# Kernel optimization log

Measured on AMD Instinct MI355X. Metric: run time of the kernel, lower is better.

Reference implementation:

```python
import jax, jax.numpy as jnp
import numpy as np

H = 8
DK = 64          # d_model // h
D_MODEL = 512
DIM_G = 64       # trignometric geometry embedding dim
WAVE_LEN = 1000.0


def box_relational_embedding(boxes):
    # boxes: [B, N, 4] = (x_min, y_min, x_max, y_max)
    x_min, y_min, x_max, y_max = [boxes[..., i:i + 1] for i in range(4)]  # each [B,N,1]
    cx = (x_min + x_max) * 0.5
    cy = (y_min + y_max) * 0.5
    w = (x_max - x_min) + 1.0
    h = (y_max - y_min) + 1.0

    def rel(c, s):
        # log(clamp(|c_i - c_j| / s_i, 1e-3)) -> [B,N,N]
        return jnp.log(jnp.clip(jnp.abs((c - jnp.swapaxes(c, -2, -1)) / s), 1e-3, None))

    delta_x = rel(cx, w)
    delta_y = rel(cy, h)
    delta_w = jnp.log(w / jnp.swapaxes(w, -2, -1))
    delta_h = jnp.log(h / jnp.swapaxes(h, -2, -1))
    pos = jnp.stack([delta_x, delta_y, delta_w, delta_h], axis=-1)  # [B,N,N,4]

    n_freq = DIM_G // 8  # 8 frequencies per geometric feature
    feat_range = jnp.arange(n_freq, dtype=pos.dtype)
    dim_mat = 1.0 / (WAVE_LEN ** (feat_range / n_freq))            # [n_freq]
    mul = (100.0 * pos)[..., None] * dim_mat                        # [B,N,N,4,n_freq]
    B, N = pos.shape[0], pos.shape[1]
    mul = mul.reshape(B, N, N, 4 * n_freq)                          # [B,N,N,32]
    return jnp.concatenate([jnp.sin(mul), jnp.cos(mul)], axis=-1)   # [B,N,N,64]


def setup_inputs() -> dict:
    key = jax.random.key(0)
    ks = jax.random.split(key, 14)
    B, N = 4, 512
    s = 0.02
    return {
        "input_query": jax.random.normal(ks[0], (B, N, D_MODEL), jnp.float32),
        "input_key":   jax.random.normal(ks[1], (B, N, D_MODEL), jnp.float32),
        "input_value": jax.random.normal(ks[2], (B, N, D_MODEL), jnp.float32),
        "input_box":   jax.random.uniform(ks[3], (B, N, 4), jnp.float32),
        "Wq": jax.random.normal(ks[4], (D_MODEL, D_MODEL), jnp.float32) * s,
        "bq": jax.random.normal(ks[5], (D_MODEL,), jnp.float32) * s,
        "Wk": jax.random.normal(ks[6], (D_MODEL, D_MODEL), jnp.float32) * s,
        "bk": jax.random.normal(ks[7], (D_MODEL,), jnp.float32) * s,
        "Wv": jax.random.normal(ks[8], (D_MODEL, D_MODEL), jnp.float32) * s,
        "bv": jax.random.normal(ks[9], (D_MODEL,), jnp.float32) * s,
        "Wo": jax.random.normal(ks[10], (D_MODEL, D_MODEL), jnp.float32) * s,
        "bo": jax.random.normal(ks[11], (D_MODEL,), jnp.float32) * s,
        "WG": jax.random.normal(ks[12], (H, DIM_G), jnp.float32) * s,
        "bG": jax.random.normal(ks[13], (H,), jnp.float32) * s,
    }


def reference(input_query, input_key, input_value, input_box,
              Wq, bq, Wk, bk, Wv, bv, Wo, bo, WG, bG):
    B, N, _ = input_query.shape

    # geometry log-bias per head: relu(Linear_h(emb)) -> [B,H,N,N]
    emb = box_relational_embedding(input_box)                        # [B,N,N,64]
    wg = jax.nn.relu(jnp.einsum('bmng,hg->bhmn', emb, WG)
                     + bG[None, :, None, None])

    def proj(x, W, b):
        # torch Linear: x @ W^T + b, then split heads -> [B,H,N,DK]
        y = x @ W.T + b
        return y.reshape(B, N, H, DK).transpose(0, 2, 1, 3)

    q = proj(input_query, Wq, bq)
    k = proj(input_key, Wk, bk)
    v = proj(input_value, Wv, bv)

    scale = 1.0 / jnp.sqrt(jnp.asarray(DK, q.dtype))
    scores = jnp.einsum('bhqd,bhkd->bhqk', q, k) * scale             # [B,H,N,N]
    logits = jnp.log(jnp.clip(wg, 1e-6, None)) + scores
    attn = jax.nn.softmax(logits, axis=-1)                           # dropout is identity in eval
    out = jnp.einsum('bhqk,bhkd->bhqd', attn, v)
    out = out.transpose(0, 2, 1, 3).reshape(B, N, H * DK)
    return out @ Wo.T + bo
```

## Files before the change

### kernel.cpp

```cpp
#include <hip/hip_runtime.h>
#include <hip/hip_bf16.h>
#include <cstdint>

typedef unsigned short u16;
typedef unsigned int u32;
typedef __attribute__((ext_vector_type(8))) short short8;
typedef __attribute__((ext_vector_type(4))) float f32x4;
typedef __attribute__((ext_vector_type(4))) unsigned int u32x4;
typedef __attribute__((ext_vector_type(4))) unsigned short u16x4;

#define REV 15.91549431f

__device__ __forceinline__ u16 f2b(float x) { return __builtin_bit_cast(u16, (__bf16)x); }
__device__ __forceinline__ u16 f2h(float x) { return __builtin_bit_cast(u16, (_Float16)x); }
__device__ __forceinline__ float c_dim_f(int f) {
    const float c[8] = {1.0f, 0.42169650f, 0.17782794f, 0.074989421f,
                        0.031622777f, 0.013335214f, 0.0056234132f, 0.0023713737f};
    return c[f];
}
__device__ __forceinline__ void gload_lds16(const void* g, void* l) {
    __builtin_amdgcn_global_load_lds((const __attribute__((address_space(1))) u32*)g,
                                     (__attribute__((address_space(3))) u32*)l, 16, 0, 0);
}

__global__ __launch_bounds__(256) void prep_k(const float* __restrict__ s0,
                                              const float* __restrict__ s1,
                                              const float* __restrict__ s2,
                                              const float* __restrict__ s3,
                                              const float* __restrict__ s4,
                                              const float* __restrict__ s5,
                                              const float* __restrict__ s6,
                                              const float* __restrict__ box,
                                              const float* __restrict__ WG,
                                              const float* __restrict__ bG,
                                              u16* __restrict__ dstX,
                                              u16* __restrict__ dstW,
                                              u16* __restrict__ outW) {
    __shared__ char embs[256 * 128];
    const int z = blockIdx.z;
    const int t = threadIdx.x;

    if (z < 7) {
        const float* s;
        u16* dst;
        if (z < 3) {
            s = (z == 0) ? s0 : (z == 1) ? s1 : s2;
            dst = dstX + (size_t)z * 1048576;
        } else {
            if (blockIdx.x >= 256) return;
            s = (z == 3) ? s3 : (z == 4) ? s4 : (z == 5) ? s5 : s6;
            dst = dstW + (size_t)(z - 3) * 262144;
        }
        int i = (blockIdx.x * 256 + t) * 4;
        float4 v = *(const float4*)&s[i];
        u16x4 o = { f2b(v.x), f2b(v.y), f2b(v.z), f2b(v.w) };
        *(u16x4*)&dst[i] = o;
        return;
    }

    const int wave = t >> 6, lane = t & 63;
    const int b = z - 7;
    const int jt = blockIdx.x & 1, ii = blockIdx.x >> 1;
    const int j = (jt << 8) + t;
    const int swz = (t & 7) << 4;

    float4 bi = *(const float4*)&box[(size_t)(((b << 9) + ii) << 2)];
    float4 bj = *(const float4*)&box[(size_t)(((b << 9) + j) << 2)];
    float cxi = (bi.x + bi.z) * 0.5f, cyi = (bi.y + bi.w) * 0.5f;
    float wdi = bi.z - bi.x + 1.0f,   hgi = bi.w - bi.y + 1.0f;
    float cxj = (bj.x + bj.z) * 0.5f, cyj = (bj.y + bj.w) * 0.5f;
    float wdj = bj.z - bj.x + 1.0f,   hgj = bj.w - bj.y + 1.0f;

    float pos[4];
    pos[0] = __logf(fmaxf(fabsf((cxi - cxj) / wdi), 1e-3f));
    pos[1] = __logf(fmaxf(fabsf((cyi - cyj) / hgi), 1e-3f));
    pos[2] = __logf(wdi) - __logf(wdj);
    pos[3] = __logf(hgi) - __logf(hgj);

#pragma unroll
    for (int p = 0; p < 4; p++) {
        float rev = pos[p] * REV;
        u32x4 sp, cp;
#pragma unroll
        for (int f = 0; f < 4; f++) {
            float a0 = rev * c_dim_f(2 * f), a1 = rev * c_dim_f(2 * f + 1);
            sp[f] = (u32)f2b(__builtin_amdgcn_sinf(a0)) | ((u32)f2b(__builtin_amdgcn_sinf(a1)) << 16);
            cp[f] = (u32)f2b(__builtin_amdgcn_cosf(a0)) | ((u32)f2b(__builtin_amdgcn_cosf(a1)) << 16);
        }
        *(u32x4*)(embs + (((t << 7) + (p << 4)) ^ swz)) = sp;
        *(u32x4*)(embs + (((t << 7) + 64 + (p << 4)) ^ swz)) = cp;
    }

    const int hh = lane & 15;
    const int ko = (lane >> 4) << 3;
    short8 bf0 = {0,0,0,0,0,0,0,0}, bf1 = {0,0,0,0,0,0,0,0};
    float bGh = 0.0f;
    if (hh < 8) {
        const float* wrow = WG + hh * 64;
#pragma unroll
        for (int e = 0; e < 8; e++) {
            bf0[e] = (short)f2b(wrow[ko + e]);
            bf1[e] = (short)f2b(wrow[32 + ko + e]);
        }
        bGh = bG[hh];
    }
    __syncthreads();

#pragma unroll
    for (int tt = 0; tt < 4; tt++) {
        int mt = (wave << 2) + tt;
        int row = (mt << 4) + hh;
        int rswz = (row & 7) << 4;
        short8 a0v = *(const short8*)(embs + (((row << 7) + (ko << 1)) ^ rswz));
        short8 a1v = *(const short8*)(embs + (((row << 7) + 64 + (ko << 1)) ^ rswz));
        f32x4 acc = {0.f, 0.f, 0.f, 0.f};
        acc = __builtin_amdgcn_mfma_f32_16x16x32_bf16(a0v, bf0, acc, 0, 0, 0);
        acc = __builtin_amdgcn_mfma_f32_16x16x32_bf16(a1v, bf1, acc, 0, 0, 0);
        if (hh < 8) {
            int j0 = (jt << 8) + (mt << 4) + ((lane >> 4) << 2);
            u16x4 ow;
#pragma unroll
            for (int r = 0; r < 4; r++)
                ow[r] = f2h(fmaxf(acc[r] + bGh, 1e-6f) * 1024.0f);
            *(u16x4*)&outW[((size_t)((b << 3) + hh) << 18) + ((size_t)ii << 9) + j0] = ow;
        }
    }
}

__global__ __launch_bounds__(256) void attn_k(const u16* __restrict__ Qb,
                                              const u16* __restrict__ Kb,
                                              const u16* __restrict__ VT,
                                              const u16* __restrict__ Wp,
                                              u16* __restrict__ ATT) {
    __shared__ u16 Pl[4][16 * 68];
    __shared__ float Mrg[3][64][25];
    const int t = threadIdx.x;
    const int wave = t >> 6, lane = t & 63;
    const int c = lane & 15, g = lane >> 4;
    const int bid = blockIdx.x;
    const int qb = bid & 31, bh = bid >> 5;
    const int b = bh >> 3, h = bh & 7;
    const int q0 = qb << 4;

    const u16* Qp = Qb + ((size_t)bh << 15);
    const u16* Kp = Kb + ((size_t)bh << 15);
    const u16* Vp = VT + ((size_t)bh << 15);
    const _Float16* Bp = (const _Float16*)Wp + ((size_t)bh << 18) + ((size_t)q0 << 9);

    short8 qf[2];
#pragma unroll
    for (int ks = 0; ks < 2; ks++)
        qf[ks] = *(const short8*)&Qp[(size_t)(q0 + c) * 64 + ks * 32 + g * 8];

    f32x4 o[4] = {};
    float m[4] = {-1e30f, -1e30f, -1e30f, -1e30f};
    float l[4] = {0.f, 0.f, 0.f, 0.f};

    for (int kt = 0; kt < 2; kt++) {
        const int k0 = ((wave << 1) + kt) << 6;
        short8 kf[4][2], vf[4][2];
#pragma unroll
        for (int jj = 0; jj < 4; jj++)
#pragma unroll
            for (int ks = 0; ks < 2; ks++) {
                kf[jj][ks] = *(const short8*)&Kp[(size_t)(k0 + jj * 16 + c) * 64 + ks * 32 + g * 8];
                vf[jj][ks] = *(const short8*)&Vp[(size_t)(jj * 16 + c) * 512 + k0 + ks * 32 + g * 8];
            }
        float wgt[4][4];
#pragma unroll
        for (int jj = 0; jj < 4; jj++)
#pragma unroll
            for (int r = 0; r < 4; r++)
                wgt[jj][r] = (float)Bp[(size_t)(g * 4 + r) * 512 + k0 + jj * 16 + c];

        f32x4 sa[4] = {};
        __builtin_amdgcn_s_setprio(1);
#pragma unroll
        for (int jj = 0; jj < 4; jj++)
#pragma unroll
            for (int ks = 0; ks < 2; ks++)
                sa[jj] = __builtin_amdgcn_mfma_f32_16x16x32_bf16(qf[ks], kf[jj][ks], sa[jj], 0, 0, 0);
        __builtin_amdgcn_s_setprio(0);

        float s[4][4];
#pragma unroll
        for (int r = 0; r < 4; r++) {
#pragma unroll
            for (int jj = 0; jj < 4; jj++)
                s[jj][r] = sa[jj][r] * 0.125f;
            float v = fmaxf(fmaxf(s[0][r], s[1][r]), fmaxf(s[2][r], s[3][r]));
#pragma unroll
            for (int off = 1; off < 16; off <<= 1)
                v = fmaxf(v, __shfl_xor(v, off));
            float mn = fmaxf(m[r], v);
            float alpha = __expf(m[r] - mn);
            m[r] = mn;
            float rs = 0.f;
#pragma unroll
            for (int jj = 0; jj < 4; jj++) {
                float p = wgt[jj][r] * __expf(s[jj][r] - mn);
                s[jj][r] = p;
                rs += p;
            }
#pragma unroll
            for (int off = 1; off < 16; off <<= 1)
                rs += __shfl_xor(rs, off);
            l[r] = l[r] * alpha + rs;
#pragma unroll
            for (int jjo = 0; jjo < 4; jjo++)
                o[jjo][r] *= alpha;
        }

#pragma unroll
        for (int jj = 0; jj < 4; jj++)
#pragma unroll
            for (int r = 0; r < 4; r++)
                Pl[wave][(g * 4 + r) * 68 + jj * 16 + c] = f2b(s[jj][r]);
        asm volatile("s_waitcnt lgkmcnt(0)" ::: "memory");
        __builtin_amdgcn_sched_barrier(0);

        short8 pa[2];
#pragma unroll
        for (int ks = 0; ks < 2; ks++)
            pa[ks] = *(const short8*)&Pl[wave][c * 68 + ks * 32 + g * 8];
        __builtin_amdgcn_s_setprio(1);
#pragma unroll
        for (int jjo = 0; jjo < 4; jjo++)
#pragma unroll
            for (int ks = 0; ks < 2; ks++)
                o[jjo] = __builtin_amdgcn_mfma_f32_16x16x32_bf16(pa[ks], vf[jjo][ks], o[jjo], 0, 0, 0);
        __builtin_amdgcn_s_setprio(0);
        __builtin_amdgcn_sched_barrier(0);
    }

    if (wave > 0) {
#pragma unroll
        for (int r = 0; r < 4; r++) {
            Mrg[wave - 1][lane][r] = m[r];
            Mrg[wave - 1][lane][4 + r] = l[r];
#pragma unroll
            for (int jjo = 0; jjo < 4; jjo++)
                Mrg[wave - 1][lane][8 + jjo * 4 + r] = o[jjo][r];
        }
    }
    __syncthreads();
    if (wave == 0) {
#pragma unroll
        for (int w = 0; w < 3; w++) {
#pragma unroll
            for (int r = 0; r < 4; r++) {
                float m1 = Mrg[w][lane][r];
                float l1 = Mrg[w][lane][4 + r];
                float mn = fmaxf(m[r], m1);
                float a0 = __expf(m[r] - mn), a1 = __expf(m1 - mn);
                m[r] = mn;
                l[r] = l[r] * a0 + l1 * a1;
#pragma unroll
                for (int jjo = 0; jjo < 4; jjo++)
                    o[jjo][r] = o[jjo][r] * a0 + Mrg[w][lane][8 + jjo * 4 + r] * a1;
            }
        }
#pragma unroll
        for (int r = 0; r < 4; r++) {
            float inv = 1.0f / l[r];
            int row = q0 + g * 4 + r;
#pragma unroll
            for (int jjo = 0; jjo < 4; jjo++)
                ATT[(size_t)(((b << 9) + row) << 9) + (h << 6) + jjo * 16 + c] = f2b(o[jjo][r] * inv);
        }
    }
}

__global__ __launch_bounds__(256) void proj_k(const u16* __restrict__ Xall,
                                              const u16* __restrict__ Wall,
                                              const float* __restrict__ bq,
                                              const float* __restrict__ bk,
                                              const float* __restrict__ bv,
                                              u16* __restrict__ Qb,
                                              u16* __restrict__ Kb,
                                              u16* __restrict__ VT) {
    __shared__ u16 As[2][64 * 32];
    __shared__ u16 Bs[2][64 * 32];

    const int t = threadIdx.x;
    const int wave = t >> 6, lane = t & 63;
    const int wr = wave >> 1, wc = wave & 1;
    const int m0 = blockIdx.y * 64, n0 = blockIdx.x * 64;
    const int z = blockIdx.z;

    const u16* A  = Xall + (size_t)z * 1048576;
    const u16* Bm = Wall + (size_t)z * 262144;
    const float* bias = (z == 0) ? bq : (z == 1) ? bk : bv;
    u16* out = (z == 0) ? Qb : (z == 1) ? Kb : VT;

    f32x4 acc[2][2] = {};
    const int srow = t >> 2;
    const int scol = (((t & 3) ^ ((t >> 3) & 3)) << 3);
    const int c = lane & 15, g = lane >> 4;
    const int gsw = (g ^ ((c >> 1) & 3)) << 3;

    const size_t arow = (size_t)(m0 + srow) * 512 + scol;
    const size_t brow = (size_t)(n0 + srow) * 512 + scol;

    gload_lds16(&A[arow], &As[0][t * 8]);
    gload_lds16(&Bm[brow], &Bs[0][t * 8]);

    int cur = 0;
    for (int k0 = 0; k0 < 512; k0 += 32, cur ^= 1) {
        if (k0 + 32 < 512) {
            gload_lds16(&A[arow + k0 + 32], &As[cur ^ 1][t * 8]);
            gload_lds16(&Bm[brow + k0 + 32], &Bs[cur ^ 1][t * 8]);
            asm volatile("s_waitcnt vmcnt(2)" ::: "memory");
        } else {
            asm volatile("s_waitcnt vmcnt(0)" ::: "memory");
        }
        __builtin_amdgcn_s_barrier();
        __builtin_amdgcn_sched_barrier(0);
        short8 af[2], bfr[2];
#pragma unroll
        for (int i = 0; i < 2; i++)
            af[i] = *(const short8*)&As[cur][(wr * 32 + i * 16 + c) * 32 + gsw];
#pragma unroll
        for (int jj = 0; jj < 2; jj++)
            bfr[jj] = *(const short8*)&Bs[cur][(wc * 32 + jj * 16 + c) * 32 + gsw];
#pragma unroll
        for (int i = 0; i < 2; i++)
#pragma unroll
            for (int jj = 0; jj < 2; jj++)
                acc[i][jj] = __builtin_amdgcn_mfma_f32_16x16x32_bf16(af[i], bfr[jj], acc[i][jj], 0, 0, 0);
        __builtin_amdgcn_sched_barrier(0);
        __builtin_amdgcn_s_barrier();
    }

#pragma unroll
    for (int i = 0; i < 2; i++)
#pragma unroll
        for (int jj = 0; jj < 2; jj++)
#pragma unroll
            for (int r = 0; r < 4; r++) {
                int row = m0 + wr * 32 + i * 16 + ((lane >> 4) << 2) + r;
                int col = n0 + wc * 32 + jj * 16 + (lane & 15);
                float v = acc[i][jj][r] + bias[col];
                int b = row >> 9, rr = row & 511, h = col >> 6, d = col & 63;
                if (z < 2)
                    out[(size_t)((((b << 3) + h) << 9) + rr) * 64 + d] = f2b(v);
                else
                    out[(size_t)((((b << 3) + h) << 6) + d) * 512 + rr] = f2b(v);
            }
}

__global__ __launch_bounds__(256) void outg_k(const u16* __restrict__ A,
                                              const u16* __restrict__ Bm,
                                              const float* __restrict__ bias,
                                              float* __restrict__ outF) {
    __shared__ u16 As[2][64 * 32];
    __shared__ u16 Bs[2][64 * 32];

    const int t = threadIdx.x;
    const int wave = t >> 6, lane = t & 63;
    const int wr = wave >> 1, wc = wave & 1;
    const int m0 = blockIdx.y * 64, n0 = blockIdx.x * 64;

    f32x4 acc[2][2] = {};
    const int srow = t >> 2;
    const int scol = (((t & 3) ^ ((t >> 3) & 3)) << 3);
    const int c = lane & 15, g = lane >> 4;
    const int gsw = (g ^ ((c >> 1) & 3)) << 3;

    const size_t arow = (size_t)(m0 + srow) * 512 + scol;
    const size_t brow = (size_t)(n0 + srow) * 512 + scol;

    gload_lds16(&A[arow], &As[0][t * 8]);
    gload_lds16(&Bm[brow], &Bs[0][t * 8]);

    int cur = 0;
    for (int k0 = 0; k0 < 512; k0 += 32, cur ^= 1) {
        if (k0 + 32 < 512) {
            gload_lds16(&A[arow + k0 + 32], &As[cur ^ 1][t * 8]);
            gload_lds16(&Bm[brow + k0 + 32], &Bs[cur ^ 1][t * 8]);
            asm volatile("s_waitcnt vmcnt(2)" ::: "memory");
        } else {
            asm volatile("s_waitcnt vmcnt(0)" ::: "memory");
        }
        __builtin_amdgcn_s_barrier();
        __builtin_amdgcn_sched_barrier(0);
        short8 af[2], bfr[2];
#pragma unroll
        for (int i = 0; i < 2; i++)
            af[i] = *(const short8*)&As[cur][(wr * 32 + i * 16 + c) * 32 + gsw];
#pragma unroll
        for (int jj = 0; jj < 2; jj++)
            bfr[jj] = *(const short8*)&Bs[cur][(wc * 32 + jj * 16 + c) * 32 + gsw];
#pragma unroll
        for (int i = 0; i < 2; i++)
#pragma unroll
            for (int jj = 0; jj < 2; jj++)
                acc[i][jj] = __builtin_amdgcn_mfma_f32_16x16x32_bf16(af[i], bfr[jj], acc[i][jj], 0, 0, 0);
        __builtin_amdgcn_sched_barrier(0);
        __builtin_amdgcn_s_barrier();
    }

#pragma unroll
    for (int i = 0; i < 2; i++)
#pragma unroll
        for (int jj = 0; jj < 2; jj++)
#pragma unroll
            for (int r = 0; r < 4; r++) {
                int row = m0 + wr * 32 + i * 16 + ((lane >> 4) << 2) + r;
                int col = n0 + wc * 32 + jj * 16 + (lane & 15);
                outF[((size_t)row << 9) + col] = acc[i][jj][r] + bias[col];
            }
}

extern "C" void kernel_launch(void* const* d_in, const int* in_sizes, int n_in,
                              void* d_out, int out_size, void* d_ws, size_t ws_size,
                              hipStream_t stream) {
    const float* inq = (const float*)d_in[0];
    const float* ink = (const float*)d_in[1];
    const float* inv = (const float*)d_in[2];
    const float* box = (const float*)d_in[3];
    const float* Wq  = (const float*)d_in[4];
    const float* bq  = (const float*)d_in[5];
    const float* Wk  = (const float*)d_in[6];
    const float* bk  = (const float*)d_in[7];
    const float* Wv  = (const float*)d_in[8];
    const float* bv  = (const float*)d_in[9];
    const float* Wo  = (const float*)d_in[10];
    const float* bo  = (const float*)d_in[11];
    const float* WG  = (const float*)d_in[12];
    const float* bG  = (const float*)d_in[13];

    u16* base = (u16*)d_ws;
    u16* Xall = base;
    u16* Wall = base + 3145728;
    u16* Qb   = base + 4194304;
    u16* Kb   = base + 5242880;
    u16* VT   = base + 6291456;
    u16* ATT  = base + 7340032;
    u16* Wp   = base + 8388608;

    prep_k<<<dim3(1024, 1, 11), 256, 0, stream>>>(inq, ink, inv, Wq, Wk, Wv, Wo,
                                                  box, WG, bG, Xall, Wall, Wp);

    proj_k<<<dim3(8, 32, 3), 256, 0, stream>>>(Xall, Wall, bq, bk, bv, Qb, Kb, VT);

    attn_k<<<dim3(1024), 256, 0, stream>>>(Qb, Kb, VT, Wp, ATT);

    outg_k<<<dim3(8, 32, 1), 256, 0, stream>>>(ATT, Wall + 786432, bo, (float*)d_out);
}
```

Baseline: 70.37 us.

## Stage geometry bias tile in LDS via async loads and batch softmax reductions

The attention kernel now copies the block's 16x512 fp16 geometry-weight tile into swizzled LDS with global_load_lds before the loop, replacing strided per-lane global gathers with LDS reads. The softmax reductions are restructured so the shuffle reductions for all four rows are interleaved, raising ILP. The P buffer is double-buffered per kt so the explicit waitcnt and sched barriers can be dropped, and the kt loop is unrolled with an occupancy hint of 3 blocks per CU. This adds 16KB of LDS per block, which may limit occupancy. Removing the explicit lgkmcnt wait relies on the compiler ordering the LDS write before the read.

New measurement: 73.62 us. +4.6%, slower.

```diff
diff --git a/kernel.cpp b/kernel.cpp
--- a/kernel.cpp
+++ b/kernel.cpp
@@ -127,12 +127,13 @@
     }
 }
 
-__global__ __launch_bounds__(256) void attn_k(const u16* __restrict__ Qb,
-                                              const u16* __restrict__ Kb,
-                                              const u16* __restrict__ VT,
-                                              const u16* __restrict__ Wp,
-                                              u16* __restrict__ ATT) {
-    __shared__ u16 Pl[4][16 * 68];
+__global__ __launch_bounds__(256, 3) void attn_k(const u16* __restrict__ Qb,
+                                                 const u16* __restrict__ Kb,
+                                                 const u16* __restrict__ VT,
+                                                 const u16* __restrict__ Wp,
+                                                 u16* __restrict__ ATT) {
+    __shared__ _Float16 Wl[16 * 512];
+    __shared__ u16 Pl[4][2][16 * 68];
     __shared__ float Mrg[3][64][25];
     const int t = threadIdx.x;
     const int wave = t >> 6, lane = t & 63;
@@ -145,7 +146,16 @@
     const u16* Qp = Qb + ((size_t)bh << 15);
     const u16* Kp = Kb + ((size_t)bh << 15);
     const u16* Vp = VT + ((size_t)bh << 15);
-    const _Float16* Bp = (const _Float16*)Wp + ((size_t)bh << 18) + ((size_t)q0 << 9);
+    const char* Bg = (const char*)(Wp + ((size_t)bh << 18) + ((size_t)q0 << 9));
+
+#pragma unroll
+    for (int p = 0; p < 4; p++) {
+        int dstb = t * 16 + p * 4096;
+        int rr = dstb >> 10;
+        int chunk = (dstb & 1023) >> 4;
+        int schunk = chunk ^ (((rr >> 2) & 3) << 1);
+        gload_lds16(Bg + rr * 1024 + schunk * 16, (char*)Wl + dstb);
+    }
 
     short8 qf[2];
 #pragma unroll
@@ -156,6 +166,9 @@
     float m[4] = {-1e30f, -1e30f, -1e30f, -1e30f};
     float l[4] = {0.f, 0.f, 0.f, 0.f};
 
+    __syncthreads();
+
+#pragma unroll
     for (int kt = 0; kt < 2; kt++) {
         const int k0 = ((wave << 1) + kt) << 6;
         short8 kf[4][2], vf[4][2];
@@ -171,7 +184,7 @@
         for (int jj = 0; jj < 4; jj++)
 #pragma unroll
             for (int r = 0; r < 4; r++)
-                wgt[jj][r] = (float)Bp[(size_t)(g * 4 + r) * 512 + k0 + jj * 16 + c];
+                wgt[jj][r] = (float)Wl[(g * 4 + r) * 512 + ((k0 + jj * 16 + c) ^ (g << 4))];
 
         f32x4 sa[4] = {};
         __builtin_amdgcn_s_setprio(1);
@@ -184,45 +197,62 @@
 
         float s[4][4];
 #pragma unroll
-        for (int r = 0; r < 4; r++) {
+        for (int r = 0; r < 4; r++)
 #pragma unroll
             for (int jj = 0; jj < 4; jj++)
                 s[jj][r] = sa[jj][r] * 0.125f;
-            float v = fmaxf(fmaxf(s[0][r], s[1][r]), fmaxf(s[2][r], s[3][r]));
-#pragma unroll
-            for (int off = 1; off < 16; off <<= 1)
-                v = fmaxf(v, __shfl_xor(v, off));
-            float mn = fmaxf(m[r], v);
-            float alpha = __expf(m[r] - mn);
+
+        float vmax[4];
+#pragma unroll
+        for (int r = 0; r < 4; r++)
+            vmax[r] = fmaxf(fmaxf(s[0][r], s[1][r]), fmaxf(s[2][r], s[3][r]));
+#pragma unroll
+        for (int off = 1; off < 16; off <<= 1)
+#pragma unroll
+            for (int r = 0; r < 4; r++)
+                vmax[r] = fmaxf(vmax[r], __shfl_xor(vmax[r], off));
+
+        float alpha[4];
+#pragma unroll
+        for (int r = 0; r < 4; r++) {
+            float mn = fmaxf(m[r], vmax[r]);
+            alpha[r] = __expf(m[r] - mn);
             m[r] = mn;
-            float rs = 0.f;
+        }
+
+        float rs[4] = {0.f, 0.f, 0.f, 0.f};
+#pragma unroll
+        for (int r = 0; r < 4; r++)
 #pragma unroll
             for (int jj = 0; jj < 4; jj++) {
-                float p = wgt[jj][r] * __expf(s[jj][r] - mn);
+                float p = wgt[jj][r] * __expf(s[jj][r] - m[r]);
                 s[jj][r] = p;
-                rs += p;
+                rs[r] += p;
             }
 #pragma unroll
-            for (int off = 1; off < 16; off <<= 1)
-                rs += __shfl_xor(rs, off);
-            l[r] = l[r] * alpha + rs;
-#pragma unroll
-            for (int jjo = 0; jjo < 4; jjo++)
-                o[jjo][r] *= alpha;
-        }
+        for (int off = 1; off < 16; off <<= 1)
+#pragma unroll
+            for (int r = 0; r < 4; r++)
+                rs[r] += __shfl_xor(rs[r], off);
+#pragma unroll
+        for (int r = 0; r < 4; r++)
+            l[r] = l[r] * alpha[r] + rs[r];
+#pragma unroll
+        for (int jjo = 0; jjo < 4; jjo++)
+#pragma unroll
+            for (int r = 0; r < 4; r++)
+                o[jjo][r] *= alpha[r];
 
 #pragma unroll
         for (int jj = 0; jj < 4; jj++)
 #pragma unroll
             for (int r = 0; r < 4; r++)
-                Pl[wave][(g * 4 + r) * 68 + jj * 16 + c] = f2b(s[jj][r]);
-        asm volatile("s_waitcnt lgkmcnt(0)" ::: "memory");
-        __builtin_amdgcn_sched_barrier(0);
+                Pl[wave][kt][(g * 4 + r) * 68 + jj * 16 + c] = f2b(s[jj][r]);
 
         short8 pa[2];
 #pragma unroll
         for (int ks = 0; ks < 2; ks++)
-            pa[ks] = *(const short8*)&Pl[wave][c * 68 + ks * 32 + g * 8];
+            pa[ks] = *(const short8*)&Pl[wave][kt][c * 68 + ks * 32 + g * 8];
         __builtin_amdgcn_s_setprio(1);
 #pragma unroll
         for (int jjo = 0; jjo < 4; jjo++)
@@ -230,7 +260,6 @@
             for (int ks = 0; ks < 2; ks++)
                 o[jjo] = __builtin_amdgcn_mfma_f32_16x16x32_bf16(pa[ks], vf[jjo][ks], o[jjo], 0, 0, 0);
         __builtin_amdgcn_s_setprio(0);
-        __builtin_amdgcn_sched_barrier(0);
     }
 
     if (wave > 0) {
```
